# Performance work log

Hardware: AMD Instinct MI355X
Metric: run time of the kernel (lower is better)

Reference implementation:

```python
import jax, jax.numpy as jnp
import numpy as np

N_NODES = 50000
N_EDGES = 500000
D_IN = 128
D_HID = 128
D_OUT = 128
N_GRAPHS = 1024


def gcn_conv(x, W, b, row, col, n_nodes):
    # x: [N, d_in] -> [N, d_out]; PyG GCNConv with add_self_loops + symmetric norm
    h = x @ W  # [N, d_out]
    loops = jnp.arange(n_nodes, dtype=row.dtype)
    r = jnp.concatenate([row, loops])  # source
    c = jnp.concatenate([col, loops])  # target
    deg = jax.ops.segment_sum(jnp.ones(r.shape[0], dtype=x.dtype), c, num_segments=n_nodes)
    dinv = jnp.where(deg > 0, jax.lax.rsqrt(jnp.maximum(deg, 1.0)), 0.0)
    norm = dinv[r] * dinv[c]  # [E+N]
    msg = h[r] * norm[:, None]  # gather + scale
    out = jax.ops.segment_sum(msg, c, num_segments=n_nodes)  # scatter-add at targets
    return out + b


def setup_inputs() -> dict:
    key = jax.random.key(0)
    ks = jax.random.split(key, 10)
    x = jax.random.normal(ks[0], (N_NODES, D_IN), dtype=jnp.float32)
    edge_index = jax.random.randint(ks[1], (2, N_EDGES), 0, N_NODES, dtype=jnp.int64)
    batch = jnp.sort(jax.random.randint(ks[2], (N_NODES,), 0, N_GRAPHS, dtype=jnp.int64))
    s1 = 1.0 / np.sqrt(D_IN)
    s2 = 1.0 / np.sqrt(D_HID)
    W1 = jax.random.uniform(ks[3], (D_IN, D_HID), jnp.float32, -s1, s1)
    b1 = jnp.zeros((D_HID,), jnp.float32)
    W2 = jax.random.uniform(ks[4], (D_HID, D_HID), jnp.float32, -s2, s2)
    b2 = jnp.zeros((D_HID,), jnp.float32)
    Wf = jax.random.uniform(ks[5], (D_HID, D_OUT), jnp.float32, -s2, s2)
    bf = jax.random.uniform(ks[6], (D_OUT,), jnp.float32, -s2, s2)
    return {"x": x, "edge_index": edge_index, "batch": batch,
            "W1": W1, "b1": b1, "W2": W2, "b2": b2, "Wf": Wf, "bf": bf}


def reference(x, edge_index, batch, W1, b1, W2, b2, Wf, bf):
    n = x.shape[0]
    row, col = edge_index[0], edge_index[1]
    h = jax.nn.relu(gcn_conv(x, W1, b1, row, col, n))
    h = jax.nn.relu(gcn_conv(h, W2, b2, row, col, n))
    # global_mean_pool over graph ids
    sums = jax.ops.segment_sum(h, batch, num_segments=N_GRAPHS)  # [G, d]
    cnts = jax.ops.segment_sum(jnp.ones((n,), h.dtype), batch, num_segments=N_GRAPHS)
    pooled = sums / jnp.maximum(cnts, 1.0)[:, None]
    return pooled @ Wf + bf  # [G, D_OUT]
```

## Files before the change

kernel.cpp:

```cpp
#include <hip/hip_runtime.h>
#include <hip/hip_bf16.h>


#define D 128

typedef __attribute__((ext_vector_type(8))) short short8;
typedef __attribute__((ext_vector_type(4))) float f32x4;

__device__ __forceinline__ int swz(int row, int kbyte) {
    return row * 256 + (kbyte ^ ((row & 7) << 4));
}

__global__ __launch_bounds__(256) void k_init(int4* __restrict__ degcnt4, int n4, int zb,
                                              int4* __restrict__ pooled4, int p4, int pb,
                                              const float* __restrict__ W1,
                                              const float* __restrict__ W2,
                                              ushort* __restrict__ h1, ushort* __restrict__ l1,
                                              ushort* __restrict__ h2, ushort* __restrict__ l2) {
    int b = blockIdx.x;
    if (b < zb) {
        int i = b * 256 + threadIdx.x;
        if (i < n4) degcnt4[i] = make_int4(0, 0, 0, 0);
        return;
    }
    if (b < zb + pb) {
        int i = (b - zb) * 256 + threadIdx.x;
        if (i < p4) pooled4[i] = make_int4(0, 0, 0, 0);
        return;
    }
    int bb = b - zb - pb;
    const float* W = (bb < 8) ? W1 : W2;
    ushort* Wh = (bb < 8) ? h1 : h2;
    ushort* Wl = (bb < 8) ? l1 : l2;
    int t = (bb & 7) * 256 + threadIdx.x;
    int nrow = t >> 4;
    int kc = t & 15;
    uint hw[8], lw[8];
#pragma unroll
    for (int j = 0; j < 8; ++j) {
        float f = W[(kc * 8 + j) * D + nrow];
        uint ub = __float_as_uint(f);
        uint hb = ub & 0xffff0000u;
        float r = f - __uint_as_float(hb);
        hw[j] = hb >> 16;
        lw[j] = __float_as_uint(r) >> 16;
    }
    uint4 vh = make_uint4(hw[0] | (hw[1] << 16), hw[2] | (hw[3] << 16),
                          hw[4] | (hw[5] << 16), hw[6] | (hw[7] << 16));
    uint4 vl = make_uint4(lw[0] | (lw[1] << 16), lw[2] | (lw[3] << 16),
                          lw[4] | (lw[5] << 16), lw[6] | (lw[7] << 16));
    *(uint4*)&Wh[nrow * D + kc * 8] = vh;
    *(uint4*)&Wl[nrow * D + kc * 8] = vl;
}

__global__ void k_deg(const int* __restrict__ col, int* __restrict__ cnt, int E) {
    int e = (blockIdx.x * blockDim.x + threadIdx.x) * 4;
    if (e + 3 < E) {
        int4 c = *(const int4*)&col[e];
        atomicAdd(&cnt[c.x], 1);
        atomicAdd(&cnt[c.y], 1);
        atomicAdd(&cnt[c.z], 1);
        atomicAdd(&cnt[c.w], 1);
    } else {
        for (; e < E; ++e) atomicAdd(&cnt[col[e]], 1);
    }
}

__global__ __launch_bounds__(256) void k_scan_partial(const int* __restrict__ cnt,
                                                      int* __restrict__ partial, int n) {
    int t = threadIdx.x;
    int base = blockIdx.x * 1024 + t * 4;
    int s = 0;
#pragma unroll
    for (int j = 0; j < 4; ++j) {
        int i = base + j;
        if (i < n) s += cnt[i];
    }
#pragma unroll
    for (int o = 32; o > 0; o >>= 1) s += __shfl_down(s, o, 64);
    __shared__ int ws[4];
    if ((t & 63) == 0) ws[t >> 6] = s;
    __syncthreads();
    if (t == 0) partial[blockIdx.x] = ws[0] + ws[1] + ws[2] + ws[3];
}

__global__ __launch_bounds__(256) void k_scan_final(const int* __restrict__ cnt,
                                                    const int* __restrict__ partial,
                                                    int* __restrict__ offs,
                                                    int* __restrict__ cursor,
                                                    float* __restrict__ dinv,
                                                    int n, int E) {
    int t = threadIdx.x;
    int lane = t & 63;
    int base = blockIdx.x * 1024 + t * 4;
    int v[4];
    int s = 0;
#pragma unroll
    for (int j = 0; j < 4; ++j) {
        int i = base + j;
        v[j] = (i < n) ? cnt[i] : 0;
        s += v[j];
    }
    int inc = s;
#pragma unroll
    for (int o = 1; o < 64; o <<= 1) {
        int u = __shfl_up(inc, o, 64);
        if (lane >= o) inc += u;
    }
    __shared__ int wsum[4];
    __shared__ int bpref;
    if (lane == 63) wsum[t >> 6] = inc;
    if (t == 0) {
        int run = 0;
        for (int b = 0; b < blockIdx.x; ++b) run += partial[b];
        bpref = run;
        if (blockIdx.x == 0) offs[n] = E;
    }
    __syncthreads();
    int woff = 0;
    int w = t >> 6;
    for (int k = 0; k < w; ++k) woff += wsum[k];
    int excl = woff + (inc - s) + bpref;
#pragma unroll
    for (int j = 0; j < 4; ++j) {
        int i = base + j;
        if (i < n) {
            offs[i] = excl;
            cursor[i] = excl;
            dinv[i] = 1.0f / sqrtf((float)(v[j] + 1));
        }
        excl += v[j];
    }
}

__global__ void k_fill(const int* __restrict__ ei, int* __restrict__ cursor,
                       int* __restrict__ csr, int E) {
    int e = (blockIdx.x * blockDim.x + threadIdx.x) * 4;
    if (e + 3 < E) {
        int4 r = *(const int4*)&ei[e];
        int4 c = *(const int4*)&ei[E + e];
        int p0 = atomicAdd(&cursor[c.x], 1);
        int p1 = atomicAdd(&cursor[c.y], 1);
        int p2 = atomicAdd(&cursor[c.z], 1);
        int p3 = atomicAdd(&cursor[c.w], 1);
        csr[p0] = r.x;
        csr[p1] = r.y;
        csr[p2] = r.z;
        csr[p3] = r.w;
    } else {
        for (; e < E; ++e) {
            int rr = ei[e], cc = ei[E + e];
            int pos = atomicAdd(&cursor[cc], 1);
            csr[pos] = rr;
        }
    }
}

#define TM 128
template <bool ASLICED>
__global__ __launch_bounds__(512, 4) void k_gemm(const float* __restrict__ A,
                                                 const ushort* __restrict__ Bt_hi,
                                                 const ushort* __restrict__ Bt_lo,
                                                 const float* __restrict__ dinv,
                                                 float* __restrict__ C, int n) {
    extern __shared__ char lds[];
    char* Bh = lds;
    char* Bl = lds + 32 * 1024;

    int tid = threadIdx.x;
    int wave = tid >> 6, lane = tid & 63;
    int li = lane & 15, lg = lane >> 4;
    int row0 = blockIdx.x * TM;
    int grow = row0 + wave * 16 + li;
    bool valid = grow < n;

    float4 a[4][2];
#pragma unroll
    for (int ks = 0; ks < 4; ++ks) {
        int k0 = ks * 32 + lg * 8;
        if (valid) {
            const float4* p;
            if (ASLICED)
                p = (const float4*)(A + ((size_t)(k0 >> 4) * n + grow) * 16 + (k0 & 15));
            else
                p = (const float4*)(A + (size_t)grow * D + k0);
            a[ks][0] = p[0];
            a[ks][1] = p[1];
        } else {
            a[ks][0] = make_float4(0.f, 0.f, 0.f, 0.f);
            a[ks][1] = make_float4(0.f, 0.f, 0.f, 0.f);
        }
    }

#pragma unroll
    for (int it = tid; it < 2048; it += 512) {
        int r = it >> 4, kc = it & 15;
        uint4 vh = *(const uint4*)(Bt_hi + r * D + kc * 8);
        uint4 vl = *(const uint4*)(Bt_lo + r * D + kc * 8);
        *(uint4*)(Bh + swz(r, kc * 16)) = vh;
        *(uint4*)(Bl + swz(r, kc * 16)) = vl;
    }
    __syncthreads();

    short8 ah[4], al[4];
#pragma unroll
    for (int ks = 0; ks < 4; ++ks) {
        float f[8] = {a[ks][0].x, a[ks][0].y, a[ks][0].z, a[ks][0].w,
                      a[ks][1].x, a[ks][1].y, a[ks][1].z, a[ks][1].w};
#pragma unroll
        for (int j = 0; j < 8; ++j) {
            uint ub = __float_as_uint(f[j]);
            uint hb = ub & 0xffff0000u;
            float r = f[j] - __uint_as_float(hb);
            ah[ks][j] = (short)(hb >> 16);
            al[ks][j] = (short)(__float_as_uint(r) >> 16);
        }
    }

    f32x4 acc[8];
#pragma unroll
    for (int i = 0; i < 8; ++i) acc[i] = (f32x4){0.f, 0.f, 0.f, 0.f};

#pragma unroll
    for (int ks = 0; ks < 4; ++ks) {
        int kb = ks * 64 + lg * 16;
#pragma unroll
        for (int nt = 0; nt < 8; ++nt) {
            short8 bh = *(const short8*)(Bh + swz(nt * 16 + li, kb));
            short8 bl = *(const short8*)(Bl + swz(nt * 16 + li, kb));
            acc[nt] = __builtin_amdgcn_mfma_f32_16x16x32_bf16(ah[ks], bh, acc[nt], 0, 0, 0);
            acc[nt] = __builtin_amdgcn_mfma_f32_16x16x32_bf16(al[ks], bh, acc[nt], 0, 0, 0);
            acc[nt] = __builtin_amdgcn_mfma_f32_16x16x32_bf16(ah[ks], bl, acc[nt], 0, 0, 0);
        }
    }

    int crow0 = row0 + wave * 16 + lg * 4;
#pragma unroll
    for (int j = 0; j < 4; ++j) {
        int gr = crow0 + j;
        if (gr < n) {
            float dv = dinv[gr];
#pragma unroll
            for (int nt = 0; nt < 8; ++nt)
                C[((size_t)nt * n + gr) * 16 + li] = acc[nt][j] * dv;
        }
    }
}

#define AGG_NB 128
#define CSR_CAP 2304
template <bool POOL>
__global__ __launch_bounds__(512) void k_agg(const float* __restrict__ hs,
                                             const float* __restrict__ dinv,
                                             const int* __restrict__ offs,
                                             const int* __restrict__ csr,
                                             const float* __restrict__ bias,
                                             float* __restrict__ outs,
                                             const int* __restrict__ batch,
                                             float* __restrict__ pooled, int n) {
    __shared__ int lofs[AGG_NB + 1];
    __shared__ int lcsr[CSR_CAP];

    int slice = blockIdx.x & 7;
    int chunk = blockIdx.x >> 3;
    int node0 = chunk * AGG_NB;
    int nend = node0 + AGG_NB; if (nend > n) nend = n;
    int nn = nend - node0;
    if ((int)threadIdx.x <= nn) lofs[threadIdx.x] = offs[node0 + threadIdx.x];
    __syncthreads();
    int S = lofs[0];
    int span = lofs[nn] - S;
    bool uselds = (span <= CSR_CAP);
    if (uselds) {
        for (int i = threadIdx.x; i < span; i += 512) lcsr[i] = csr[S + i];
    }
    __syncthreads();

    int lnode = threadIdx.x >> 2;
    int node = node0 + lnode;
    bool act = node < n;
    int l4q = threadIdx.x & 3;
    int l4 = l4q * 4;

    const float* hbase = hs + (size_t)slice * n * 16;
    f32x4 v = (f32x4){0.f, 0.f, 0.f, 0.f};
    if (act) {
        float di = dinv[node];
        int s = lofs[lnode] - S, e = lofs[lnode + 1] - S;
        f32x4 acc = *(const f32x4*)(hbase + (size_t)node * 16 + l4);
        if (uselds) {
            int p = s;
            for (; p + 8 <= e; p += 8) {
                int r0 = lcsr[p],     r1 = lcsr[p + 1], r2 = lcsr[p + 2], r3 = lcsr[p + 3];
                int r4 = lcsr[p + 4], r5 = lcsr[p + 5], r6 = lcsr[p + 6], r7 = lcsr[p + 7];
                f32x4 h0 = *(const f32x4*)(hbase + (size_t)r0 * 16 + l4);
                f32x4 h1 = *(const f32x4*)(hbase + (size_t)r1 * 16 + l4);
                f32x4 h2 = *(const f32x4*)(hbase + (size_t)r2 * 16 + l4);
                f32x4 h3 = *(const f32x4*)(hbase + (size_t)r3 * 16 + l4);
                f32x4 h4 = *(const f32x4*)(hbase + (size_t)r4 * 16 + l4);
                f32x4 h5 = *(const f32x4*)(hbase + (size_t)r5 * 16 + l4);
                f32x4 h6 = *(const f32x4*)(hbase + (size_t)r6 * 16 + l4);
                f32x4 h7 = *(const f32x4*)(hbase + (size_t)r7 * 16 + l4);
                acc += ((h0 + h1) + (h2 + h3)) + ((h4 + h5) + (h6 + h7));
            }
            for (; p + 4 <= e; p += 4) {
                int r0 = lcsr[p], r1 = lcsr[p + 1], r2 = lcsr[p + 2], r3 = lcsr[p + 3];
                f32x4 h0 = *(const f32x4*)(hbase + (size_t)r0 * 16 + l4);
                f32x4 h1 = *(const f32x4*)(hbase + (size_t)r1 * 16 + l4);
                f32x4 h2 = *(const f32x4*)(hbase + (size_t)r2 * 16 + l4);
                f32x4 h3 = *(const f32x4*)(hbase + (size_t)r3 * 16 + l4);
                acc += (h0 + h1) + (h2 + h3);
            }
            for (; p < e; ++p)
                acc += *(const f32x4*)(hbase + (size_t)lcsr[p] * 16 + l4);
        } else {
            const int* gcsr = csr + S;
            int p = s;
            for (; p + 4 <= e; p += 4) {
                int r0 = gcsr[p], r1 = gcsr[p + 1], r2 = gcsr[p + 2], r3 = gcsr[p + 3];
                f32x4 h0 = *(const f32x4*)(hbase + (size_t)r0 * 16 + l4);
                f32x4 h1 = *(const f32x4*)(hbase + (size_t)r1 * 16 + l4);
                f32x4 h2 = *(const f32x4*)(hbase + (size_t)r2 * 16 + l4);
                f32x4 h3 = *(const f32x4*)(hbase + (size_t)r3 * 16 + l4);
                acc += (h0 + h1) + (h2 + h3);
            }
            for (; p < e; ++p)
                acc += *(const f32x4*)(hbase + (size_t)gcsr[p] * 16 + l4);
        }
        f32x4 b4 = *(const f32x4*)(bias + slice * 16 + l4);
#pragma unroll
        for (int j = 0; j < 4; ++j) v[j] = fmaxf(acc[j] * di + b4[j], 0.f);
    }

    if constexpr (!POOL) {
        if (act)
            __builtin_nontemporal_store(v, (f32x4*)(outs + ((size_t)slice * n + node) * 16 + l4));
    } else {
        int g = act ? batch[node] : -1;
        int lane = threadIdx.x & 63;
#pragma unroll
        for (int o = 4; o <= 32; o <<= 1) {
            f32x4 ov;
            ov[0] = __shfl_down(v[0], o, 64);
            ov[1] = __shfl_down(v[1], o, 64);
            ov[2] = __shfl_down(v[2], o, 64);
            ov[3] = __shfl_down(v[3], o, 64);
            int og = __shfl_down(g, o, 64);
            if ((lane + o) < 64 && og == g) v += ov;
        }
        int pg = __shfl_up(g, 4, 64);
        if (act && (lane < 4 || pg != g)) {
            float* pp = pooled + (size_t)g * D + slice * 16 + l4;
            atomicAdd(pp + 0, v[0]);
            atomicAdd(pp + 1, v[1]);
            atomicAdd(pp + 2, v[2]);
            atomicAdd(pp + 3, v[3]);
        }
    }
}

__global__ __launch_bounds__(128) void k_final(const float* __restrict__ pooled,
                                               const int* __restrict__ batch, int n,
                                               const float* __restrict__ Wf,
                                               const float* __restrict__ bf,
                                               float* __restrict__ out) {
    __shared__ int sse[2];
    __shared__ float pr[D];
    int g = blockIdx.x;
    if (threadIdx.x == 0) {
        int lo = 0, hi = n;
        while (lo < hi) { int m = (lo + hi) >> 1; if (batch[m] < g) lo = m + 1; else hi = m; }
        sse[0] = lo;
    } else if (threadIdx.x == 64) {
        int lo = 0, hi = n;
        while (lo < hi) { int m = (lo + hi) >> 1; if (batch[m] < g + 1) lo = m + 1; else hi = m; }
        sse[1] = lo;
    }
    __syncthreads();
    float cnt = (float)(sse[1] - sse[0]);
    if (cnt < 1.f) cnt = 1.f;
    int d = threadIdx.x;
    pr[d] = pooled[(size_t)g * D + d] / cnt;
    __syncthreads();
    float o = bf[d];
#pragma unroll 8
    for (int k = 0; k < D; ++k) o += pr[k] * Wf[k * D + d];
    out[g * D + d] = o;
}

extern "C" void kernel_launch(void* const* d_in, const int* in_sizes, int n_in,
                              void* d_out, int out_size, void* d_ws, size_t ws_size,
                              hipStream_t stream) {
    const float* x  = (const float*)d_in[0];
    const int*   ei = (const int*)d_in[1];
    const int*   bt = (const int*)d_in[2];
    const float* W1 = (const float*)d_in[3];
    const float* b1 = (const float*)d_in[4];
    const float* W2 = (const float*)d_in[5];
    const float* b2 = (const float*)d_in[6];
    const float* Wf = (const float*)d_in[7];
    const float* bf = (const float*)d_in[8];
    float* out = (float*)d_out;

    int n = in_sizes[2];
    int E = in_sizes[1] / 2;
    int G = out_size / D;

    char* w = (char*)d_ws;
    size_t off = 0;
    auto alloc = [&](size_t bytes) -> void* {
        void* p = w + off;
        off = (off + bytes + 511) & ~(size_t)511;
        return p;
    };
    int*    degcnt = (int*)alloc((size_t)n * 4);
    int*    cursor = (int*)alloc((size_t)n * 4);
    int*    offs   = (int*)alloc((size_t)(n + 1) * 4);
    float*  dinv   = (float*)alloc((size_t)n * 4);
    int*    csr    = (int*)alloc((size_t)E * 4);
    float*  hw     = (float*)alloc((size_t)n * D * 4);
    float*  ha     = (float*)alloc((size_t)n * D * 4);
    float*  pooled = (float*)alloc((size_t)G * D * 4);
    int*    partial= (int*)alloc((size_t)256 * 4);
    ushort* wt1h   = (ushort*)alloc((size_t)D * D * 2);
    ushort* wt1l   = (ushort*)alloc((size_t)D * D * 2);
    ushort* wt2h   = (ushort*)alloc((size_t)D * D * 2);
    ushort* wt2l   = (ushort*)alloc((size_t)D * D * 2);

    int n4 = (n + 3) / 4;
    int zb = (n4 + 255) / 256;
    int p4 = (G * D + 3) / 4;
    int pb = (p4 + 255) / 256;
    k_init<<<zb + pb + 16, 256, 0, stream>>>((int4*)degcnt, n4, zb,
                                             (int4*)pooled, p4, pb,
                                             W1, W2, wt1h, wt1l, wt2h, wt2l);

    int e4b = (E / 4 + 255) / 256 + 1;
    int sb = (n + 1023) / 1024;
    k_deg<<<e4b, 256, 0, stream>>>(ei + E, degcnt, E);
    k_scan_partial<<<sb, 256, 0, stream>>>(degcnt, partial, n);
    k_scan_final<<<sb, 256, 0, stream>>>(degcnt, partial, offs, cursor, dinv, n, E);
    k_fill<<<e4b, 256, 0, stream>>>(ei, cursor, csr, E);

    int gb = (n + TM - 1) / TM;
    int ab = 8 * ((n + AGG_NB - 1) / AGG_NB);
    size_t lds_bytes = 64 * 1024;

    k_gemm<false><<<gb, 512, lds_bytes, stream>>>(x, wt1h, wt1l, dinv, hw, n);
    k_agg<false><<<ab, 512, 0, stream>>>(hw, dinv, offs, csr, b1, ha, bt, nullptr, n);
    k_gemm<true><<<gb, 512, lds_bytes, stream>>>(ha, wt2h, wt2l, dinv, hw, n);
    k_agg<true><<<ab, 512, 0, stream>>>(hw, dinv, offs, csr, b2, nullptr, bt, pooled, n);
    k_final<<<G, 128, 0, stream>>>(pooled, bt, n, Wf, bf, out);
}
```

Baseline: 163.5 us.

## Fuse CSR-building prep kernels into one cooperative kernel with grid syncs

Replaces five separate preprocessing launches (init, degree count, two-pass scan, CSR fill) with one cooperative kernel of 256 blocks that uses grid.sync between phases. The scan computes each block's prefix by summing all earlier degree counts directly instead of using a partials buffer. This is meant to remove launch gaps between the small kernels. The cost is fewer resident blocks for the atomic-heavy phases and redundant prefix reads. The GEMM output stores are also changed to nontemporal stores.

```diff
diff --git a/kernel.cpp b/kernel.cpp
--- a/kernel.cpp
+++ b/kernel.cpp
@@ -1,5 +1,8 @@
 #include <hip/hip_runtime.h>
 #include <hip/hip_bf16.h>
+#include <hip/hip_cooperative_groups.h>
+
+namespace cg = cooperative_groups;
 
 
 #define D 128
@@ -11,132 +14,117 @@
     return row * 256 + (kbyte ^ ((row & 7) << 4));
 }
 
-__global__ __launch_bounds__(256) void k_init(int4* __restrict__ degcnt4, int n4, int zb,
-                                              int4* __restrict__ pooled4, int p4, int pb,
+__global__ __launch_bounds__(256) void k_prep(int* __restrict__ degcnt,
+                                              int* __restrict__ offs,
+                                              int* __restrict__ cursor,
+                                              float* __restrict__ dinv,
+                                              float* __restrict__ pooled,
+                                              const int* __restrict__ ei,
+                                              int* __restrict__ csr,
                                               const float* __restrict__ W1,
                                               const float* __restrict__ W2,
                                               ushort* __restrict__ h1, ushort* __restrict__ l1,
-                                              ushort* __restrict__ h2, ushort* __restrict__ l2) {
-    int b = blockIdx.x;
-    if (b < zb) {
-        int i = b * 256 + threadIdx.x;
-        if (i < n4) degcnt4[i] = make_int4(0, 0, 0, 0);
-        return;
-    }
-    if (b < zb + pb) {
-        int i = (b - zb) * 256 + threadIdx.x;
-        if (i < p4) pooled4[i] = make_int4(0, 0, 0, 0);
-        return;
-    }
-    int bb = b - zb - pb;
-    const float* W = (bb < 8) ? W1 : W2;
-    ushort* Wh = (bb < 8) ? h1 : h2;
-    ushort* Wl = (bb < 8) ? l1 : l2;
-    int t = (bb & 7) * 256 + threadIdx.x;
-    int nrow = t >> 4;
-    int kc = t & 15;
-    uint hw[8], lw[8];
-#pragma unroll
-    for (int j = 0; j < 8; ++j) {
-        float f = W[(kc * 8 + j) * D + nrow];
-        uint ub = __float_as_uint(f);
-        uint hb = ub & 0xffff0000u;
-        float r = f - __uint_as_float(hb);
-        hw[j] = hb >> 16;
-        lw[j] = __float_as_uint(r) >> 16;
-    }
-    uint4 vh = make_uint4(hw[0] | (hw[1] << 16), hw[2] | (hw[3] << 16),
-                          hw[4] | (hw[5] << 16), hw[6] | (hw[7] << 16));
-    uint4 vl = make_uint4(lw[0] | (lw[1] << 16), lw[2] | (lw[3] << 16),
-                          lw[4] | (lw[5] << 16), lw[6] | (lw[7] << 16));
-    *(uint4*)&Wh[nrow * D + kc * 8] = vh;
-    *(uint4*)&Wl[nrow * D + kc * 8] = vl;
-}
-
-__global__ void k_deg(const int* __restrict__ col, int* __restrict__ cnt, int E) {
-    int e = (blockIdx.x * blockDim.x + threadIdx.x) * 4;
-    if (e + 3 < E) {
-        int4 c = *(const int4*)&col[e];
-        atomicAdd(&cnt[c.x], 1);
-        atomicAdd(&cnt[c.y], 1);
-        atomicAdd(&cnt[c.z], 1);
-        atomicAdd(&cnt[c.w], 1);
-    } else {
-        for (; e < E; ++e) atomicAdd(&cnt[col[e]], 1);
-    }
-}
-
-__global__ __launch_bounds__(256) void k_scan_partial(const int* __restrict__ cnt,
-                                                      int* __restrict__ partial, int n) {
-    int t = threadIdx.x;
-    int base = blockIdx.x * 1024 + t * 4;
-    int s = 0;
-#pragma unroll
-    for (int j = 0; j < 4; ++j) {
-        int i = base + j;
-        if (i < n) s += cnt[i];
-    }
-#pragma unroll
-    for (int o = 32; o > 0; o >>= 1) s += __shfl_down(s, o, 64);
-    __shared__ int ws[4];
-    if ((t & 63) == 0) ws[t >> 6] = s;
-    __syncthreads();
-    if (t == 0) partial[blockIdx.x] = ws[0] + ws[1] + ws[2] + ws[3];
-}
-
-__global__ __launch_bounds__(256) void k_scan_final(const int* __restrict__ cnt,
-                                                    const int* __restrict__ partial,
-                                                    int* __restrict__ offs,
-                                                    int* __restrict__ cursor,
-                                                    float* __restrict__ dinv,
-                                                    int n, int E) {
-    int t = threadIdx.x;
-    int lane = t & 63;
-    int base = blockIdx.x * 1024 + t * 4;
-    int v[4];
-    int s = 0;
-#pragma unroll
-    for (int j = 0; j < 4; ++j) {
-        int i = base + j;
-        v[j] = (i < n) ? cnt[i] : 0;
-        s += v[j];
-    }
-    int inc = s;
-#pragma unroll
-    for (int o = 1; o < 64; o <<= 1) {
-        int u = __shfl_up(inc, o, 64);
-        if (lane >= o) inc += u;
-    }
-    __shared__ int wsum[4];
-    __shared__ int bpref;
-    if (lane == 63) wsum[t >> 6] = inc;
-    if (t == 0) {
-        int run = 0;
-        for (int b = 0; b < blockIdx.x; ++b) run += partial[b];
-        bpref = run;
-        if (blockIdx.x == 0) offs[n] = E;
-    }
-    __syncthreads();
-    int woff = 0;
-    int w = t >> 6;
-    for (int k = 0; k < w; ++k) woff += wsum[k];
-    int excl = woff + (inc - s) + bpref;
-#pragma unroll
-    for (int j = 0; j < 4; ++j) {
-        int i = base + j;
-        if (i < n) {
-            offs[i] = excl;
-            cursor[i] = excl;
-            dinv[i] = 1.0f / sqrtf((float)(v[j] + 1));
-        }
-        excl += v[j];
-    }
-}
-
-__global__ void k_fill(const int* __restrict__ ei, int* __restrict__ cursor,
-                       int* __restrict__ csr, int E) {
-    int e = (blockIdx.x * blockDim.x + threadIdx.x) * 4;
-    if (e + 3 < E) {
+                                              ushort* __restrict__ h2, ushort* __restrict__ l2,
+                                              int n, int E, int G) {
+    cg::grid_group grid = cg::this_grid();
+    int gtid = blockIdx.x * 256 + threadIdx.x;
+    int gsz = gridDim.x * 256;
+
+    for (int i = gtid; i < n; i += gsz) degcnt[i] = 0;
+    for (int i = gtid; i < G * D; i += gsz) pooled[i] = 0.f;
+    for (int t = gtid; t < 4096; t += gsz) {
+        int bb = t >> 11;
+        int tt = t & 2047;
+        const float* W = bb ? W2 : W1;
+        ushort* Wh = bb ? h2 : h1;
+        ushort* Wl = bb ? l2 : l1;
+        int nrow = tt >> 4;
+        int kc = tt & 15;
+        uint hw[8], lw[8];
+#pragma unroll
+        for (int j = 0; j < 8; ++j) {
+            float f = W[(kc * 8 + j) * D + nrow];
+            uint ub = __float_as_uint(f);
+            uint hb = ub & 0xffff0000u;
+            float r = f - __uint_as_float(hb);
+            hw[j] = hb >> 16;
+            lw[j] = __float_as_uint(r) >> 16;
+        }
+        uint4 vh = make_uint4(hw[0] | (hw[1] << 16), hw[2] | (hw[3] << 16),
+                              hw[4] | (hw[5] << 16), hw[6] | (hw[7] << 16));
+        uint4 vl = make_uint4(lw[0] | (lw[1] << 16), lw[2] | (lw[3] << 16),
+                              lw[4] | (lw[5] << 16), lw[6] | (lw[7] << 16));
+        *(uint4*)&Wh[nrow * D + kc * 8] = vh;
+        *(uint4*)&Wl[nrow * D + kc * 8] = vl;
+    }
+    grid.sync();
+
+    const int* col = ei + E;
+    int nq = E >> 2;
+    for (int q = gtid; q < nq; q += gsz) {
+        int4 c = ((const int4*)col)[q];
+        atomicAdd(&degcnt[c.x], 1);
+        atomicAdd(&degcnt[c.y], 1);
+        atomicAdd(&degcnt[c.z], 1);
+        atomicAdd(&degcnt[c.w], 1);
+    }
+    for (int e = (nq << 2) + gtid; e < E; e += gsz) atomicAdd(&degcnt[col[e]], 1);
+    grid.sync();
+
+    if (blockIdx.x * 1024 < n) {
+        int c = blockIdx.x;
+        int t = threadIdx.x;
+        int lane = t & 63;
+        int ps = 0;
+        for (int i = t; i < c * 1024; i += 256) ps += degcnt[i];
+#pragma unroll
+        for (int o = 32; o > 0; o >>= 1) ps += __shfl_down(ps, o, 64);
+        __shared__ int ws2[4];
+        __shared__ int bpref;
+        if (lane == 0) ws2[t >> 6] = ps;
+        __syncthreads();
+        if (t == 0) {
+            bpref = ws2[0] + ws2[1] + ws2[2] + ws2[3];
+            if (c == 0) offs[n] = E;
+        }
+        __syncthreads();
+        int base = c * 1024 + t * 4;
+        int v[4];
+        int s = 0;
+#pragma unroll
+        for (int j = 0; j < 4; ++j) {
+            int i = base + j;
+            v[j] = (i < n) ? degcnt[i] : 0;
+            s += v[j];
+        }
+        int inc = s;
+#pragma unroll
+        for (int o = 1; o < 64; o <<= 1) {
+            int u = __shfl_up(inc, o, 64);
+            if (lane >= o) inc += u;
+        }
+        __shared__ int wsum[4];
+        if (lane == 63) wsum[t >> 6] = inc;
+        __syncthreads();
+        int woff = 0;
+        int w = t >> 6;
+        for (int k = 0; k < w; ++k) woff += wsum[k];
+        int excl = woff + (inc - s) + bpref;
+#pragma unroll
+        for (int j = 0; j < 4; ++j) {
+            int i = base + j;
+            if (i < n) {
+                offs[i] = excl;
+                cursor[i] = excl;
+                dinv[i] = 1.0f / sqrtf((float)(v[j] + 1));
+            }
+            excl += v[j];
+        }
+    }
+    grid.sync();
+
+    for (int q = gtid; q < nq; q += gsz) {
+        int e = q << 2;
         int4 r = *(const int4*)&ei[e];
         int4 c = *(const int4*)&ei[E + e];
         int p0 = atomicAdd(&cursor[c.x], 1);
@@ -147,12 +135,11 @@
         csr[p1] = r.y;
         csr[p2] = r.z;
         csr[p3] = r.w;
-    } else {
-        for (; e < E; ++e) {
-            int rr = ei[e], cc = ei[E + e];
-            int pos = atomicAdd(&cursor[cc], 1);
-            csr[pos] = rr;
-        }
+    }
+    for (int e = (nq << 2) + gtid; e < E; e += gsz) {
+        int rr = ei[e], cc = ei[E + e];
+        int pos = atomicAdd(&cursor[cc], 1);
+        csr[pos] = rr;
     }
 }
 
@@ -242,7 +229,8 @@
             float dv = dinv[gr];
 #pragma unroll
             for (int nt = 0; nt < 8; ++nt)
-                C[((size_t)nt * n + gr) * 16 + li] = acc[nt][j] * dv;
+                __builtin_nontemporal_store(acc[nt][j] * dv,
+                                            &C[((size_t)nt * n + gr) * 16 + li]);
         }
     }
 }
@@ -421,26 +409,19 @@
     float*  hw     = (float*)alloc((size_t)n * D * 4);
     float*  ha     = (float*)alloc((size_t)n * D * 4);
     float*  pooled = (float*)alloc((size_t)G * D * 4);
-    int*    partial= (int*)alloc((size_t)256 * 4);
     ushort* wt1h   = (ushort*)alloc((size_t)D * D * 2);
     ushort* wt1l   = (ushort*)alloc((size_t)D * D * 2);
     ushort* wt2h   = (ushort*)alloc((size_t)D * D * 2);
     ushort* wt2l   = (ushort*)alloc((size_t)D * D * 2);
 
-    int n4 = (n + 3) / 4;
-    int zb = (n4 + 255) / 256;
-    int p4 = (G * D + 3) / 4;
-    int pb = (p4 + 255) / 256;
-    k_init<<<zb + pb + 16, 256, 0, stream>>>((int4*)degcnt, n4, zb,
-                                             (int4*)pooled, p4, pb,
-                                             W1, W2, wt1h, wt1l, wt2h, wt2l);
-
-    int e4b = (E / 4 + 255) / 256 + 1;
-    int sb = (n + 1023) / 1024;
-    k_deg<<<e4b, 256, 0, stream>>>(ei + E, degcnt, E);
-    k_scan_partial<<<sb, 256, 0, stream>>>(degcnt, partial, n);
-    k_scan_final<<<sb, 256, 0, stream>>>(degcnt, partial, offs, cursor, dinv, n, E);
-    k_fill<<<e4b, 256, 0, stream>>>(ei, cursor, csr, E);
+    {
+        void* args[] = {(void*)&degcnt, (void*)&offs, (void*)&cursor, (void*)&dinv,
+                        (void*)&pooled, (void*)&ei, (void*)&csr,
+                        (void*)&W1, (void*)&W2,
+                        (void*)&wt1h, (void*)&wt1l, (void*)&wt2h, (void*)&wt2l,
+                        (void*)&n, (void*)&E, (void*)&G};
+        hipLaunchCooperativeKernel((void*)k_prep, dim3(256), dim3(256), args, 0, stream);
+    }
 
     int gb = (n + TM - 1) / TM;
     int ab = 8 * ((n + AGG_NB - 1) / AGG_NB);
```

Result: slower. 272.9 us (+66.9%).
